# Performance work log

Hardware: AMD Instinct MI355X
Metric: run time of the kernel (lower is better)

The kernel has to match this reference:

```python
import jax, jax.numpy as jnp
import numpy as np

B, S, D_MODEL, H = 2, 2048, 1024, 16
DEPTH = D_MODEL // H


def setup_inputs() -> dict:
    key = jax.random.key(0)
    ks = jax.random.split(key, 12)
    s = 1.0 / np.sqrt(D_MODEL)
    inp = {
        "q": jax.random.normal(ks[0], (B, S, D_MODEL), jnp.float32),
        "k": jax.random.normal(ks[1], (B, S, D_MODEL), jnp.float32),
        "v": jax.random.normal(ks[2], (B, S, D_MODEL), jnp.float32),
        # CTRL-style causal mask: 1 where position is disallowed (future), 0 otherwise
        "mask": jnp.triu(jnp.ones((S, S), jnp.float32), k=1),
        "Wq_w": jax.random.normal(ks[3], (D_MODEL, D_MODEL), jnp.float32) * s,
        "Wq_b": jax.random.normal(ks[4], (D_MODEL,), jnp.float32) * s,
        "Wk_w": jax.random.normal(ks[5], (D_MODEL, D_MODEL), jnp.float32) * s,
        "Wk_b": jax.random.normal(ks[6], (D_MODEL,), jnp.float32) * s,
        "Wv_w": jax.random.normal(ks[7], (D_MODEL, D_MODEL), jnp.float32) * s,
        "Wv_b": jax.random.normal(ks[8], (D_MODEL,), jnp.float32) * s,
        "dense_w": jax.random.normal(ks[9], (D_MODEL, D_MODEL), jnp.float32) * s,
        "dense_b": jax.random.normal(ks[10], (D_MODEL,), jnp.float32) * s,
    }
    return inp


def _split_heads(x):
    # [B, S, D] -> [B, H, S, depth]
    b, s, _ = x.shape
    return x.reshape(b, s, H, DEPTH).transpose(0, 2, 1, 3)


def reference(q, k, v, mask, Wq_w, Wq_b, Wk_w, Wk_b, Wv_w, Wv_b, dense_w, dense_b):
    b = q.shape[0]
    # torch Linear: y = x @ W^T + b
    qh = _split_heads(q @ Wq_w.T + Wq_b)  # [B,H,Sq,dh]
    kh = _split_heads(k @ Wk_w.T + Wk_b)  # [B,H,Sk,dh]
    vh = _split_heads(v @ Wv_w.T + Wv_b)  # [B,H,Sk,dh]

    scale = 1.0 / np.sqrt(DEPTH)
    logits = jnp.einsum("bhqd,bhkd->bhqk", qh, kh) * scale  # [B,H,Sq,Sk]
    nd, ns = logits.shape[-2], logits.shape[-1]
    logits = logits + mask[ns - nd:ns, :ns] * -10000.0
    attn = jax.nn.softmax(logits, axis=-1)
    ctx = jnp.einsum("bhqk,bhkd->bhqd", attn, vh)  # [B,H,Sq,dh]
    ctx = ctx.transpose(0, 2, 1, 3).reshape(b, -1, D_MODEL)  # [B,Sq,D]
    out = ctx @ dense_w.T + dense_b
    return out
```

## Files before the change

### kernel.cpp

```cpp
#include <hip/hip_runtime.h>
#include <hip/hip_bf16.h>

typedef __bf16 bf16x8 __attribute__((ext_vector_type(8)));
typedef __bf16 bf16x4 __attribute__((ext_vector_type(4)));
typedef float  f32x4  __attribute__((ext_vector_type(4)));

#define D_MODEL 1024
#define SEQ     2048
#define NH      16
#define DH      64
#define MTOT    4096

__device__ __forceinline__ void gload16(const void* gp, void* lp) {
  __builtin_amdgcn_global_load_lds(
      (const __attribute__((address_space(1))) unsigned int*)gp,
      (__attribute__((address_space(3))) unsigned int*)lp,
      16, 0, 0);
}

struct CvtSegs {
  const float* s[7];
  __bf16*      d[7];
  int          n8[7];
};

__global__ __launch_bounds__(256) void cvt_kernel(CvtSegs c) {
  const int seg = blockIdx.y;
  const float4* s = (const float4*)c.s[seg];
  bf16x8*       d = (bf16x8*)c.d[seg];
  const int n8 = c.n8[seg];
  for (int i = blockIdx.x * 256 + threadIdx.x; i < n8; i += gridDim.x * 256) {
    float4 a = s[2 * i];
    float4 b = s[2 * i + 1];
    bf16x8 o;
    o[0] = (__bf16)a.x; o[1] = (__bf16)a.y; o[2] = (__bf16)a.z; o[3] = (__bf16)a.w;
    o[4] = (__bf16)b.x; o[5] = (__bf16)b.y; o[6] = (__bf16)b.z; o[7] = (__bf16)b.w;
    d[i] = o;
  }
}

template <int EPI>
__device__ __forceinline__ void gemm_core(const __bf16* __restrict__ A,
                                          const __bf16* __restrict__ W,
                                          const float* __restrict__ bias,
                                          void* __restrict__ outp,
                                          __bf16* Asm, __bf16* Bsm,
                                          int row0, int col0) {
  const int tid = threadIdx.x;
  const int lane = tid & 63;
  const int w = tid >> 6;
  const int lr = lane & 15, lg = lane >> 4;
  const int wr = w >> 1, wc = w & 1;
  char* AsB = (char*)Asm;
  char* BsB = (char*)Bsm;

  f32x4 acc[4][4];
#pragma unroll
  for (int i = 0; i < 4; ++i)
#pragma unroll
    for (int j = 0; j < 4; ++j) acc[i][j] = (f32x4){0.f, 0.f, 0.f, 0.f};

  for (int k0 = 0; k0 < D_MODEL; k0 += 64) {
#pragma unroll
    for (int i = 0; i < 4; ++i) {
      const int c0 = i * 4 + w;
      const int bo = c0 * 1024 + lane * 16;
      const int row = bo >> 7;
      const int gch = ((bo >> 4) & 7) ^ (row & 7);
      gload16(A + (size_t)(row0 + row) * D_MODEL + k0 + gch * 8, AsB + c0 * 1024);
      gload16(W + (size_t)(col0 + row) * D_MODEL + k0 + gch * 8, BsB + c0 * 1024);
    }
    __syncthreads();
#pragma unroll
    for (int kk = 0; kk < 2; ++kk) {
      bf16x8 af[4], bfr[4];
      const int kc = kk * 4 + lg;
#pragma unroll
      for (int mi = 0; mi < 4; ++mi) {
        const int row = wr * 64 + mi * 16 + lr;
        af[mi] = *(const bf16x8*)(AsB + row * 128 + ((kc ^ (row & 7)) << 4));
      }
#pragma unroll
      for (int ni = 0; ni < 4; ++ni) {
        const int col = wc * 64 + ni * 16 + lr;
        bfr[ni] = *(const bf16x8*)(BsB + col * 128 + ((kc ^ (col & 7)) << 4));
      }
#pragma unroll
      for (int mi = 0; mi < 4; ++mi)
#pragma unroll
        for (int ni = 0; ni < 4; ++ni)
          acc[mi][ni] = __builtin_amdgcn_mfma_f32_16x16x32_bf16(af[mi], bfr[ni],
                                                                acc[mi][ni], 0, 0, 0);
    }
    __syncthreads();
  }

  if (EPI == 2) {
    __bf16* o = (__bf16*)outp;
#pragma unroll
    for (int mi = 0; mi < 4; ++mi) {
#pragma unroll
      for (int ni = 0; ni < 4; ++ni) {
        const int n = col0 + wc * 64 + ni * 16 + lr;
        const float bv = bias[n];
        const int m0 = row0 + wr * 64 + mi * 16 + lg * 4;
        bf16x4 pk;
#pragma unroll
        for (int j = 0; j < 4; ++j) pk[j] = (__bf16)(acc[mi][ni][j] + bv);
        *(bf16x4*)(o + ((size_t)((m0 >> 11) * NH + (n >> 6)) * DH + (n & 63)) * SEQ +
                   (m0 & 2047)) = pk;
      }
    }
  } else {
#pragma unroll
    for (int mi = 0; mi < 4; ++mi) {
#pragma unroll
      for (int ni = 0; ni < 4; ++ni) {
        const int n = col0 + wc * 64 + ni * 16 + lr;
        const float bv = bias[n];
#pragma unroll
        for (int j = 0; j < 4; ++j) {
          const int m = row0 + wr * 64 + mi * 16 + lg * 4 + j;
          const float v = acc[mi][ni][j] + bv;
          if (EPI == 0) {
            __bf16* o = (__bf16*)outp;
            o[(size_t)((m >> 11) * NH + (n >> 6)) * (SEQ * DH) +
              (size_t)(m & 2047) * DH + (n & 63)] = (__bf16)v;
          } else {
            float* o = (float*)outp;
            o[(size_t)m * D_MODEL + n] = v;
          }
        }
      }
    }
  }
}

struct QkvPtrs {
  const __bf16* A[3];
  const __bf16* W[3];
  const float*  b[3];
  __bf16*       o[3];
};

__global__ __launch_bounds__(256) void gemm_qkv_kernel(QkvPtrs p) {
  __shared__ __bf16 As[128 * 64];
  __shared__ __bf16 Bs[128 * 64];
  const int z = blockIdx.z;
  if (z == 2)
    gemm_core<2>(p.A[z], p.W[z], p.b[z], p.o[z], As, Bs,
                 blockIdx.x * 128, blockIdx.y * 128);
  else
    gemm_core<0>(p.A[z], p.W[z], p.b[z], p.o[z], As, Bs,
                 blockIdx.x * 128, blockIdx.y * 128);
}

__global__ __launch_bounds__(256) void gemm_out_kernel(const __bf16* __restrict__ A,
                                                       const __bf16* __restrict__ W,
                                                       const float* __restrict__ b,
                                                       float* __restrict__ o) {
  __shared__ __bf16 As[128 * 64];
  __shared__ __bf16 Bs[128 * 64];
  gemm_core<1>(A, W, b, o, As, Bs, blockIdx.x * 128, blockIdx.y * 128);
}

__global__ __launch_bounds__(256, 4) void attn_kernel(const __bf16* __restrict__ qh,
                                                      const __bf16* __restrict__ kh,
                                                      const __bf16* __restrict__ vt,
                                                      __bf16* __restrict__ ctx) {
  __shared__ __bf16 Ks[2][64 * 64];
  __shared__ __bf16 Vt[2][64 * 64];
  __shared__ __bf16 Ps[4][16 * 64];

  const int bh = blockIdx.x;
  const int qb = 31 - blockIdx.y;
  const int tid = threadIdx.x, lane = tid & 63, w = tid >> 6;
  const int lr = lane & 15, lg = lane >> 4;
  const size_t hoff = (size_t)bh * SEQ * DH;
  const __bf16* Q   = qh + hoff;
  const __bf16* Kp  = kh + hoff;
  const __bf16* Vtp = vt + hoff;
  const int q0 = qb * 64 + w * 16;

  bf16x8 qf[2];
#pragma unroll
  for (int ki = 0; ki < 2; ++ki)
    qf[ki] = *(const bf16x8*)(Q + (size_t)(q0 + lr) * DH + ki * 32 + lg * 8);

  f32x4 o[4];
#pragma unroll
  for (int ni = 0; ni < 4; ++ni) o[ni] = (f32x4){0.f, 0.f, 0.f, 0.f};
  float lsum = 0.f;

  char* Psw = (char*)Ps[w];
  const int nt = qb + 1;

#pragma unroll
  for (int s = 0; s < 2; ++s) {
    const int c = (w * 2 + s) * 64 + lane;
    const int row = c >> 3;
    const int gch = (c & 7) ^ (row & 7);
    gload16(Kp + (size_t)row * DH + gch * 8, (char*)Ks[0] + (w * 2 + s) * 1024);
    gload16(Vtp + (size_t)row * SEQ + gch * 8, (char*)Vt[0] + (w * 2 + s) * 1024);
  }

  int cur = 0;
  for (int t = 0; t < nt; ++t) {
    __syncthreads();
    if (t + 1 < nt) {
      const int nxt = cur ^ 1;
#pragma unroll
      for (int s = 0; s < 2; ++s) {
        const int c = (w * 2 + s) * 64 + lane;
        const int row = c >> 3;
        const int gch = (c & 7) ^ (row & 7);
        gload16(Kp + (size_t)((t + 1) * 64 + row) * DH + gch * 8,
                (char*)Ks[nxt] + (w * 2 + s) * 1024);
        gload16(Vtp + (size_t)row * SEQ + (t + 1) * 64 + gch * 8,
                (char*)Vt[nxt] + (w * 2 + s) * 1024);
      }
    }
    {
      char* KsB = (char*)Ks[cur];
      char* VtB = (char*)Vt[cur];

      f32x4 st[4];
#pragma unroll
      for (int ni = 0; ni < 4; ++ni) st[ni] = (f32x4){0.f, 0.f, 0.f, 0.f};
      __builtin_amdgcn_s_setprio(1);
#pragma unroll
      for (int ki = 0; ki < 2; ++ki) {
        const int kc = ki * 4 + lg;
#pragma unroll
        for (int ni = 0; ni < 4; ++ni) {
          const int row = ni * 16 + lr;
          bf16x8 kf = *(const bf16x8*)(KsB + row * 128 + ((kc ^ (row & 7)) << 4));
          st[ni] = __builtin_amdgcn_mfma_f32_16x16x32_bf16(kf, qf[ki], st[ni], 0, 0, 0);
        }
      }
      __builtin_amdgcn_s_setprio(0);

      const int kvb = t * 64;
      const bool needmask = (kvb + 63 > q0);
      const int q = q0 + lr;
      float p[4][4];
      float psum = 0.f;
#pragma unroll
      for (int ni = 0; ni < 4; ++ni) {
#pragma unroll
        for (int j = 0; j < 4; ++j) {
          float v = st[ni][j] * 0.18033688f;
          if (needmask && (kvb + ni * 16 + lg * 4 + j > q)) v = -1e9f;
          const float pe = __builtin_amdgcn_exp2f(v);
          p[ni][j] = pe;
          psum += pe;
        }
      }
      lsum += psum;

#pragma unroll
      for (int ni = 0; ni < 4; ++ni) {
        bf16x4 pk;
#pragma unroll
        for (int j = 0; j < 4; ++j) pk[j] = (__bf16)p[ni][j];
        const int chunk = 2 * ni + (lg >> 1);
        *(bf16x4*)(Psw + lr * 128 + ((chunk ^ (lr & 7)) << 4) + (lg & 1) * 8) = pk;
      }
      asm volatile("s_waitcnt lgkmcnt(0)" ::: "memory");
      __builtin_amdgcn_sched_barrier(0);

      __builtin_amdgcn_s_setprio(1);
#pragma unroll
      for (int ki = 0; ki < 2; ++ki) {
        const int kc = ki * 4 + lg;
        bf16x8 pf2 = *(const bf16x8*)(Psw + lr * 128 + ((kc ^ (lr & 7)) << 4));
#pragma unroll
        for (int ni = 0; ni < 4; ++ni) {
          const int d = ni * 16 + lr;
          bf16x8 vf = *(const bf16x8*)(VtB + d * 128 + ((kc ^ (lr & 7)) << 4));
          o[ni] = __builtin_amdgcn_mfma_f32_16x16x32_bf16(pf2, vf, o[ni], 0, 0, 0);
        }
      }
      __builtin_amdgcn_s_setprio(0);
    }
    cur ^= 1;
  }

  lsum += __shfl_xor(lsum, 16, 64);
  lsum += __shfl_xor(lsum, 32, 64);
  const int bb = bh >> 4, hh = bh & 15;
#pragma unroll
  for (int j = 0; j < 4; ++j) {
    const int row = lg * 4 + j;
    const float inv = 1.0f / __shfl(lsum, row, 64);
    const int qrow = q0 + row;
    __bf16* orow = ctx + (size_t)(bb * SEQ + qrow) * D_MODEL + hh * DH;
#pragma unroll
    for (int ni = 0; ni < 4; ++ni)
      orow[ni * 16 + lr] = (__bf16)(o[ni][j] * inv);
  }
}

extern "C" void kernel_launch(void* const* d_in, const int* in_sizes, int n_in,
                              void* d_out, int out_size, void* d_ws, size_t ws_size,
                              hipStream_t stream) {
  (void)in_sizes; (void)n_in; (void)out_size; (void)ws_size;
  const float* q  = (const float*)d_in[0];
  const float* k  = (const float*)d_in[1];
  const float* v  = (const float*)d_in[2];
  const float* Wq = (const float*)d_in[4];
  const float* bq = (const float*)d_in[5];
  const float* Wk = (const float*)d_in[6];
  const float* bk = (const float*)d_in[7];
  const float* Wv = (const float*)d_in[8];
  const float* bv = (const float*)d_in[9];
  const float* Wd = (const float*)d_in[10];
  const float* bd = (const float*)d_in[11];

  char* ws = (char*)d_ws;
  __bf16* qb  = (__bf16*)(ws + 0);
  __bf16* kb  = (__bf16*)(ws + 8388608);
  __bf16* vb  = (__bf16*)(ws + 16777216);
  __bf16* wqb = (__bf16*)(ws + 25165824);
  __bf16* wkb = (__bf16*)(ws + 27262976);
  __bf16* wvb = (__bf16*)(ws + 29360128);
  __bf16* wdb = (__bf16*)(ws + 31457280);
  __bf16* qhp = (__bf16*)(ws + 33554432);
  __bf16* khp = (__bf16*)(ws + 41943040);
  __bf16* vtp = (__bf16*)(ws + 50331648);
  __bf16* ctxp= (__bf16*)(ws + 58720256);

  CvtSegs cs;
  cs.s[0] = q;  cs.d[0] = qb;  cs.n8[0] = 524288;
  cs.s[1] = k;  cs.d[1] = kb;  cs.n8[1] = 524288;
  cs.s[2] = v;  cs.d[2] = vb;  cs.n8[2] = 524288;
  cs.s[3] = Wq; cs.d[3] = wqb; cs.n8[3] = 131072;
  cs.s[4] = Wk; cs.d[4] = wkb; cs.n8[4] = 131072;
  cs.s[5] = Wv; cs.d[5] = wvb; cs.n8[5] = 131072;
  cs.s[6] = Wd; cs.d[6] = wdb; cs.n8[6] = 131072;
  cvt_kernel<<<dim3(256, 7, 1), dim3(256), 0, stream>>>(cs);

  QkvPtrs qp;
  qp.A[0] = qb;  qp.A[1] = kb;  qp.A[2] = vb;
  qp.W[0] = wqb; qp.W[1] = wkb; qp.W[2] = wvb;
  qp.b[0] = bq;  qp.b[1] = bk;  qp.b[2] = bv;
  qp.o[0] = qhp; qp.o[1] = khp; qp.o[2] = vtp;
  gemm_qkv_kernel<<<dim3(32, 8, 3), dim3(256), 0, stream>>>(qp);

  attn_kernel<<<dim3(32, 32, 1), dim3(256), 0, stream>>>(qhp, khp, vtp, ctxp);

  gemm_out_kernel<<<dim3(32, 8, 1), dim3(256), 0, stream>>>(ctxp, wdb, bd, (float*)d_out);
}
```

Baseline: 123.5 us.

## Double-buffer GEMM LDS tiles with K=32 steps and raise MFMA priority

The GEMM main loop now uses two LDS buffers of 128x32 tiles. The next K-slice is prefetched via global_load_lds while the current one is consumed, and there is one barrier per iteration instead of two. The XOR swizzle is dropped in favour of a plain 64-byte row layout, and s_setprio is raised around the MFMA block. The aim is to hide global-load latency behind compute, at the cost of more iterations, and possible LDS bank conflicts now that the swizzle is gone.

```diff
diff --git a/kernel.cpp b/kernel.cpp
--- a/kernel.cpp
+++ b/kernel.cpp
@@ -60,39 +60,52 @@
 #pragma unroll
     for (int j = 0; j < 4; ++j) acc[i][j] = (f32x4){0.f, 0.f, 0.f, 0.f};
 
-  for (int k0 = 0; k0 < D_MODEL; k0 += 64) {
-#pragma unroll
-    for (int i = 0; i < 4; ++i) {
-      const int c0 = i * 4 + w;
-      const int bo = c0 * 1024 + lane * 16;
-      const int row = bo >> 7;
-      const int gch = ((bo >> 4) & 7) ^ (row & 7);
-      gload16(A + (size_t)(row0 + row) * D_MODEL + k0 + gch * 8, AsB + c0 * 1024);
-      gload16(W + (size_t)(col0 + row) * D_MODEL + k0 + gch * 8, BsB + c0 * 1024);
-    }
+  const int kch = (lane & 3) * 8;
+
+#pragma unroll
+  for (int s = 0; s < 2; ++s) {
+    const int cb = (w * 2 + s) * 64;
+    const int arow = (cb + lane) >> 2;
+    gload16(A + (size_t)(row0 + arow) * D_MODEL + kch, AsB + cb * 16);
+    gload16(W + (size_t)(col0 + arow) * D_MODEL + kch, BsB + cb * 16);
+  }
+
+  int cur = 0;
+  for (int t = 0; t < 32; ++t) {
     __syncthreads();
-#pragma unroll
-    for (int kk = 0; kk < 2; ++kk) {
+    if (t + 1 < 32) {
+      const int nxt = cur ^ 1;
+      const int k0 = (t + 1) * 32;
+#pragma unroll
+      for (int s = 0; s < 2; ++s) {
+        const int cb = (w * 2 + s) * 64;
+        const int arow = (cb + lane) >> 2;
+        gload16(A + (size_t)(row0 + arow) * D_MODEL + k0 + kch,
+                AsB + nxt * 8192 + cb * 16);
+        gload16(W + (size_t)(col0 + arow) * D_MODEL + k0 + kch,
+                BsB + nxt * 8192 + cb * 16);
+      }
+    }
+    {
+      char* Ab = AsB + cur * 8192;
+      char* Bb = BsB + cur * 8192;
       bf16x8 af[4], bfr[4];
-      const int kc = kk * 4 + lg;
-#pragma unroll
-      for (int mi = 0; mi < 4; ++mi) {
-        const int row = wr * 64 + mi * 16 + lr;
-        af[mi] = *(const bf16x8*)(AsB + row * 128 + ((kc ^ (row & 7)) << 4));
-      }
-#pragma unroll
-      for (int ni = 0; ni < 4; ++ni) {
-        const int col = wc * 64 + ni * 16 + lr;
-        bfr[ni] = *(const bf16x8*)(BsB + col * 128 + ((kc ^ (col & 7)) << 4));
-      }
+#pragma unroll
+      for (int mi = 0; mi < 4; ++mi)
+        af[mi] = *(const bf16x8*)(Ab + (wr * 64 + mi * 16 + lr) * 64 + lg * 16);
+#pragma unroll
+      for (int ni = 0; ni < 4; ++ni)
+        bfr[ni] = *(const bf16x8*)(Bb + (wc * 64 + ni * 16 + lr) * 64 + lg * 16);
+      __builtin_amdgcn_s_setprio(1);
 #pragma unroll
       for (int mi = 0; mi < 4; ++mi)
 #pragma unroll
         for (int ni = 0; ni < 4; ++ni)
           acc[mi][ni] = __builtin_amdgcn_mfma_f32_16x16x32_bf16(af[mi], bfr[ni],
                                                                 acc[mi][ni], 0, 0, 0);
-    }
-    __syncthreads();
+      __builtin_amdgcn_s_setprio(0);
+    }
+    cur ^= 1;
   }
 
   if (EPI == 2) {
@@ -144,14 +157,14 @@
 };
 
 __global__ __launch_bounds__(256) void gemm_qkv_kernel(QkvPtrs p) {
-  __shared__ __bf16 As[128 * 64];
-  __shared__ __bf16 Bs[128 * 64];
+  __shared__ __bf16 As[2][128 * 32];
+  __shared__ __bf16 Bs[2][128 * 32];
   const int z = blockIdx.z;
   if (z == 2)
-    gemm_core<2>(p.A[z], p.W[z], p.b[z], p.o[z], As, Bs,
+    gemm_core<2>(p.A[z], p.W[z], p.b[z], p.o[z], &As[0][0], &Bs[0][0],
                  blockIdx.x * 128, blockIdx.y * 128);
   else
-    gemm_core<0>(p.A[z], p.W[z], p.b[z], p.o[z], As, Bs,
+    gemm_core<0>(p.A[z], p.W[z], p.b[z], p.o[z], &As[0][0], &Bs[0][0],
                  blockIdx.x * 128, blockIdx.y * 128);
 }
 
@@ -159,9 +172,9 @@
                                                        const __bf16* __restrict__ W,
                                                        const float* __restrict__ b,
                                                        float* __restrict__ o) {
-  __shared__ __bf16 As[128 * 64];
-  __shared__ __bf16 Bs[128 * 64];
-  gemm_core<1>(A, W, b, o, As, Bs, blockIdx.x * 128, blockIdx.y * 128);
+  __shared__ __bf16 As[2][128 * 32];
+  __shared__ __bf16 Bs[2][128 * 32];
+  gemm_core<1>(A, W, b, o, &As[0][0], &Bs[0][0], blockIdx.x * 128, blockIdx.y * 128);
 }
 
 __global__ __launch_bounds__(256, 4) void attn_kernel(const __bf16* __restrict__ qh,
```

Result: faster. 120.0 us (-2.9%).
